# Kernel tuning notes

Measured on AMD Instinct MI355X. Metric: run time of the kernel, lower is better.

Reference implementation:

```python
import jax, jax.numpy as jnp
import numpy as np

EMBED_DIM = 768
Q_DIM = 64
V_DIM = 64
WINDOW_SIZE = 3


def setup_inputs() -> dict:
    key = jax.random.key(0)
    ks = jax.random.split(key, 7)
    B, N = 4, 4096
    s = 1.0 / np.sqrt(EMBED_DIM)
    x = jax.random.normal(ks[0], (B, N, EMBED_DIM), dtype=jnp.float32)
    Wq = jax.random.normal(ks[1], (EMBED_DIM, Q_DIM), dtype=jnp.float32) * s
    bq = jax.random.normal(ks[2], (Q_DIM,), dtype=jnp.float32) * 0.01
    Wk = jax.random.normal(ks[3], (EMBED_DIM, Q_DIM), dtype=jnp.float32) * s
    bk = jax.random.normal(ks[4], (Q_DIM,), dtype=jnp.float32) * 0.01
    Wv = jax.random.normal(ks[5], (EMBED_DIM, V_DIM), dtype=jnp.float32) * s
    bv = jax.random.normal(ks[6], (V_DIM,), dtype=jnp.float32) * 0.01
    return {"x": x, "Wq": Wq, "bq": bq, "Wk": Wk, "bk": bk, "Wv": Wv, "bv": bv}


def reference(x, Wq, bq, Wk, bk, Wv, bv):
    # Faithful translation of SliddingWindowAttention.forward, including the
    # original's quirk: diagonal scores are written into columns 0..window_size-1
    # of a full (B, N, N) zero matrix, softmax is taken over ALL N columns
    # (zeros included), and the result is matmul'd with V.
    B, N, _ = x.shape
    Q = x @ Wq + bq  # (B, N, Q_DIM)
    K = x @ Wk + bk  # (B, N, Q_DIM)
    V = x @ Wv + bv  # (B, N, V_DIM)

    half = WINDOW_SIZE // 2
    columns = jnp.zeros((B, N, N), dtype=x.dtype)
    for idx, di in enumerate(range(-half, half + 1)):
        # diagonal offset di: pair row i with column j = i + di (valid rows only)
        rows = np.arange(max(0, -di), N - max(0, di))
        cols_j = rows + di
        c = jnp.einsum('bid,bid->bi', Q[:, rows, :], K[:, cols_j, :])
        columns = columns.at[:, rows, idx].set(c)

    attn = jax.nn.softmax(columns, axis=2)  # (B, N, N)
    return attn @ V  # (B, N, V_DIM)
```

## Files before the change

kernel.cpp:

```cpp
#include <hip/hip_runtime.h>
#include <math.h>

#define EMBED 768
#define NTOK  4096
#define NB    4
#define ROWS  16384
#define CN    192

typedef __attribute__((ext_vector_type(8))) short bf16x8;
typedef __attribute__((ext_vector_type(8))) unsigned short u16x8;
typedef __attribute__((ext_vector_type(4))) float f32x4;

__device__ inline void split2(float f, short& h, short& l) {
  union { float f; unsigned u; } a; a.f = f;
  unsigned r = (a.u + 0x7FFFu + ((a.u >> 16) & 1u)) & 0xFFFF0000u;
  h = (short)(r >> 16);
  union { unsigned u; float f; } hf; hf.u = r;
  union { float f; unsigned u; } b; b.f = f - hf.f;
  l = (short)((b.u + 0x7FFFu + ((b.u >> 16) & 1u)) >> 16);
}

__device__ inline void splitA(float f, short& h, short& l) {
  union { float f; unsigned u; } a; a.f = f;
  unsigned r = (a.u + 0x7FFFu + ((a.u >> 16) & 1u)) & 0xFFFF0000u;
  h = (short)(r >> 16);
  union { unsigned u; float f; } hf; hf.u = r;
  union { float f; unsigned u; } b; b.f = f - hf.f;
  l = (short)((b.u + 0x8000u) >> 16);
}

__global__ __launch_bounds__(256) void wprep(const float* __restrict__ Wq,
                                             const float* __restrict__ Wk,
                                             const float* __restrict__ Wv,
                                             unsigned short* __restrict__ Wt,
                                             float* __restrict__ Vsum) {
  __shared__ float tile[32 * 64];
  const int b   = blockIdx.x;
  const int mat = b / 24;
  const int ks  = b - mat * 24;
  const float* W = (mat == 0) ? Wq : (mat == 1) ? Wk : Wv;
  const int t = threadIdx.x;

  const float4* src = (const float4*)(W + ks * 2048);
  ((float4*)tile)[t]       = src[t];
  ((float4*)tile)[t + 256] = src[t + 256];
  __syncthreads();

  const int n  = t >> 2;
  const int ko = (t & 3) * 8;
  u16x8 hv, lv;
#pragma unroll
  for (int j = 0; j < 8; ++j) {
    short h, l;
    split2(tile[(ko + j) * 64 + n], h, l);
    hv[j] = (unsigned short)h;
    lv[j] = (unsigned short)l;
  }
  const size_t base = (size_t)ks * 12288 + (size_t)(mat * 64 + n) * 32 + ko;
  *(u16x8*)(Wt + base)        = hv;
  *(u16x8*)(Wt + base + 6144) = lv;

  if (b == 0 && t < NB * 64) Vsum[t] = 0.f;
}

__device__ inline void gload_lds16(const unsigned short* g, unsigned short* l) {
  __builtin_amdgcn_global_load_lds(
      (const __attribute__((address_space(1))) unsigned int*)(g),
      (__attribute__((address_space(3))) unsigned int*)(l),
      16, 0, 0);
}

#define STAGE(LB, KS) do {                                            \
    const unsigned short* _g = Wtu + (size_t)(KS) * 12288 + tid * 8;  \
    unsigned short* _l = (LB) + tid * 8;                              \
    gload_lds16(_g,          _l);                                     \
    gload_lds16(_g + 2048,   _l + 2048);                              \
    gload_lds16(_g + 4096,   _l + 4096);                              \
    gload_lds16(_g + 6144,   _l + 6144);                              \
    gload_lds16(_g + 8192,   _l + 8192);                              \
    gload_lds16(_g + 10240,  _l + 10240);                             \
  } while (0)

#define DO_NT(LBP, NT, ACC) do {                                               \
    bf16x8 _bh = *(const bf16x8*)((LBP) + (NT) * 512);                         \
    bf16x8 _bl = *(const bf16x8*)((LBP) + (NT) * 512 + 6144);                  \
    ACC = __builtin_amdgcn_mfma_f32_16x16x32_bf16(ah, _bh, ACC, 0, 0, 0);      \
    ACC = __builtin_amdgcn_mfma_f32_16x16x32_bf16(ah, _bl, ACC, 0, 0, 0);      \
    ACC = __builtin_amdgcn_mfma_f32_16x16x32_bf16(al, _bh, ACC, 0, 0, 0);      \
  } while (0)

#define COMPUTE(LB, F0, F1) do {                                      \
    bf16x8 ah, al; short _h, _l;                                      \
    splitA((F0).x, _h, _l); ah[0] = _h; al[0] = _l;                   \
    splitA((F0).y, _h, _l); ah[1] = _h; al[1] = _l;                   \
    splitA((F0).z, _h, _l); ah[2] = _h; al[2] = _l;                   \
    splitA((F0).w, _h, _l); ah[3] = _h; al[3] = _l;                   \
    splitA((F1).x, _h, _l); ah[4] = _h; al[4] = _l;                   \
    splitA((F1).y, _h, _l); ah[5] = _h; al[5] = _l;                   \
    splitA((F1).z, _h, _l); ah[6] = _h; al[6] = _l;                   \
    splitA((F1).w, _h, _l); ah[7] = _h; al[7] = _l;                   \
    const unsigned short* _lb = (LB) + lboff;                         \
    DO_NT(_lb, 0, acc0); DO_NT(_lb, 1, acc1); DO_NT(_lb, 2, acc2);    \
    DO_NT(_lb, 3, acc3); DO_NT(_lb, 4, acc4); DO_NT(_lb, 5, acc5);    \
  } while (0)

__global__ __launch_bounds__(256, 2) void qkv_mfma(const float* __restrict__ x,
                                                   const unsigned short* __restrict__ Wtu,
                                                   const float* __restrict__ bq,
                                                   const float* __restrict__ bk,
                                                   const float* __restrict__ bv,
                                                   float* __restrict__ C,
                                                   float* __restrict__ Vsum) {
  __shared__ unsigned short lbuf0[12288];
  __shared__ unsigned short lbuf1[12288];

  const int tid   = threadIdx.x;
  const int lane  = tid & 63;
  const int wm    = (tid >> 6) & 1;
  const int wn    = tid >> 7;
  const int ml    = lane & 15;
  const int q     = lane >> 4;
  const int r0    = blockIdx.x * 32;
  const int nbase = wn * 96;
  const int lboff = (wn * 96 + ml) * 32 + q * 8;

  f32x4 acc0 = {0.f, 0.f, 0.f, 0.f}, acc1 = {0.f, 0.f, 0.f, 0.f},
        acc2 = {0.f, 0.f, 0.f, 0.f}, acc3 = {0.f, 0.f, 0.f, 0.f},
        acc4 = {0.f, 0.f, 0.f, 0.f}, acc5 = {0.f, 0.f, 0.f, 0.f};

  const float* xap = x + (size_t)(r0 + wm * 16 + ml) * EMBED + q * 8;

  STAGE(lbuf0, 0);
  float4 a0 = *(const float4*)xap;
  float4 a1 = *(const float4*)(xap + 4);

  for (int ks = 0; ks < 24; ks += 2) {
    __syncthreads();
    STAGE(lbuf1, ks + 1);
    float4 n0 = *(const float4*)(xap + 32);
    float4 n1 = *(const float4*)(xap + 36);
    COMPUTE(lbuf0, a0, a1);

    __syncthreads();
    if (ks < 22) {
      STAGE(lbuf0, ks + 2);
      float4 m0 = *(const float4*)(xap + 64);
      float4 m1 = *(const float4*)(xap + 68);
      a0 = m0; a1 = m1;
    }
    COMPUTE(lbuf1, n0, n1);
    xap += 64;
  }

#define EPI(NT, ACC) do {                                                   \
    const int n = nbase + (NT) * 16 + ml;                                   \
    const float bias = (n < 64) ? bq[n] : (n < 128) ? bk[n - 64] : bv[n - 128]; \
    const int row = r0 + wm * 16 + q * 4;                                   \
    C[(size_t)(row + 0) * CN + n] = ACC[0] + bias;                          \
    C[(size_t)(row + 1) * CN + n] = ACC[1] + bias;                          \
    C[(size_t)(row + 2) * CN + n] = ACC[2] + bias;                          \
    C[(size_t)(row + 3) * CN + n] = ACC[3] + bias;                          \
  } while (0)

  EPI(0, acc0); EPI(1, acc1); EPI(2, acc2);
  EPI(3, acc3); EPI(4, acc4); EPI(5, acc5);

#define VS(NT, ACC) do {                                                    \
    const int n = nbase + (NT) * 16 + ml;                                   \
    float s = ACC[0] + ACC[1] + ACC[2] + ACC[3] + 4.f * bv[n - 128];        \
    s += __shfl_xor(s, 16, 64);                                             \
    s += __shfl_xor(s, 32, 64);                                             \
    if (q == 0) atomicAdd(&Vsum[(r0 >> 12) * 64 + (n - 128)], s);           \
  } while (0)

  if (wn == 1) {
    VS(2, acc2); VS(3, acc3); VS(4, acc4); VS(5, acc5);
  }
}

__global__ __launch_bounds__(256) void attn_kernel(const float* __restrict__ C,
                                                   const float* __restrict__ Vsum,
                                                   float* __restrict__ out) {
  const int t    = threadIdx.x;
  const int lane = t & 63;
  const int wave = t >> 6;
  const int r = blockIdx.x * 4 + wave;
  const int b = r >> 12;
  const int i = r & (NTOK - 1);

  const float q  = C[(size_t)r * CN + lane];
  const float kc = C[(size_t)r * CN + 64 + lane];
  float km = 0.f, kp = 0.f;
  if (i > 0)        km = C[(size_t)(r - 1) * CN + 64 + lane];
  if (i < NTOK - 1) kp = C[(size_t)(r + 1) * CN + 64 + lane];

  float p0 = q * km, p1 = q * kc, p2 = q * kp;
#pragma unroll
  for (int off = 32; off > 0; off >>= 1) {
    p0 += __shfl_xor(p0, off, 64);
    p1 += __shfl_xor(p1, off, 64);
    p2 += __shfl_xor(p2, off, 64);
  }

  const float s0 = (i > 0) ? p0 : 0.f;
  const float s1 = p1;
  const float s2 = (i < NTOK - 1) ? p2 : 0.f;
  const float m  = fmaxf(fmaxf(s0, s1), fmaxf(s2, 0.f));
  const float e0 = expf(s0 - m);
  const float e1 = expf(s1 - m);
  const float e2 = expf(s2 - m);
  const float ez = expf(-m);
  const float Z  = e0 + e1 + e2 + (float)(NTOK - 3) * ez;

  const size_t vb = ((size_t)b * NTOK) * CN + 128;
  const float v0 = C[vb + lane];
  const float v1 = C[vb + CN + lane];
  const float v2 = C[vb + 2 * (size_t)CN + lane];
  const float vs = Vsum[b * 64 + lane];

  out[(size_t)r * 64 + lane] =
      (e0 * v0 + e1 * v1 + e2 * v2 + ez * (vs - v0 - v1 - v2)) / Z;
}

extern "C" void kernel_launch(void* const* d_in, const int* in_sizes, int n_in,
                              void* d_out, int out_size, void* d_ws, size_t ws_size,
                              hipStream_t stream) {
  const float* x  = (const float*)d_in[0];
  const float* Wq = (const float*)d_in[1];
  const float* bq = (const float*)d_in[2];
  const float* Wk = (const float*)d_in[3];
  const float* bk = (const float*)d_in[4];
  const float* Wv = (const float*)d_in[5];
  const float* bv = (const float*)d_in[6];
  float* out = (float*)d_out;

  float* C    = (float*)d_ws;
  float* Vsum = C + (size_t)ROWS * CN;
  unsigned short* Wt = (unsigned short*)(Vsum + NB * 64);

  wprep<<<72, 256, 0, stream>>>(Wq, Wk, Wv, Wt, Vsum);
  qkv_mfma<<<512, 256, 0, stream>>>(x, Wt, bq, bk, bv, C, Vsum);
  attn_kernel<<<ROWS / 4, 256, 0, stream>>>(C, Vsum, out);
}
```

Before: 128.2 us.

## Re-tile QKV MFMA warps across N, reuse B fragments, use hardware bf16 split

Changes the QKV projection's warp tiling. Each of the 4 waves now covers all 32 rows and 48 output columns, instead of a 2x2 split of 16 rows by 96 columns. Each B fragment loaded from LDS is reused across two A fragments, which roughly halves B LDS reads per MFMA. The weight layout in wprep is reorganized to suit the new LDS offsets. The float-to-bf16 hi/lo split now uses the HIP bf16 conversion intrinsics, with different rounding for the low part than the custom splitA. In exchange, each lane now does twice the x loads and conversions.

```diff
diff --git a/kernel.cpp b/kernel.cpp
--- a/kernel.cpp
+++ b/kernel.cpp
@@ -1,4 +1,5 @@
 #include <hip/hip_runtime.h>
+#include <hip/hip_bf16.h>
 #include <math.h>
 
 #define EMBED 768
@@ -18,15 +19,6 @@
   union { unsigned u; float f; } hf; hf.u = r;
   union { float f; unsigned u; } b; b.f = f - hf.f;
   l = (short)((b.u + 0x7FFFu + ((b.u >> 16) & 1u)) >> 16);
-}
-
-__device__ inline void splitA(float f, short& h, short& l) {
-  union { float f; unsigned u; } a; a.f = f;
-  unsigned r = (a.u + 0x7FFFu + ((a.u >> 16) & 1u)) & 0xFFFF0000u;
-  h = (short)(r >> 16);
-  union { unsigned u; float f; } hf; hf.u = r;
-  union { float f; unsigned u; } b; b.f = f - hf.f;
-  l = (short)((b.u + 0x8000u) >> 16);
 }
 
 __global__ __launch_bounds__(256) void wprep(const float* __restrict__ Wq,
@@ -46,17 +38,17 @@
   ((float4*)tile)[t + 256] = src[t + 256];
   __syncthreads();
 
-  const int n  = t >> 2;
-  const int ko = (t & 3) * 8;
+  const int q    = t >> 6;
+  const int nloc = t & 63;
   u16x8 hv, lv;
 #pragma unroll
   for (int j = 0; j < 8; ++j) {
     short h, l;
-    split2(tile[(ko + j) * 64 + n], h, l);
+    split2(tile[(q * 8 + j) * 64 + nloc], h, l);
     hv[j] = (unsigned short)h;
     lv[j] = (unsigned short)l;
   }
-  const size_t base = (size_t)ks * 12288 + (size_t)(mat * 64 + n) * 32 + ko;
+  const size_t base = (size_t)ks * 12288 + (size_t)q * 1536 + (size_t)(mat * 64 + nloc) * 8;
   *(u16x8*)(Wt + base)        = hv;
   *(u16x8*)(Wt + base + 6144) = lv;
 
@@ -81,27 +73,45 @@
     gload_lds16(_g + 10240,  _l + 10240);                             \
   } while (0)
 
-#define DO_NT(LBP, NT, ACC) do {                                               \
-    bf16x8 _bh = *(const bf16x8*)((LBP) + (NT) * 512);                         \
-    bf16x8 _bl = *(const bf16x8*)((LBP) + (NT) * 512 + 6144);                  \
-    ACC = __builtin_amdgcn_mfma_f32_16x16x32_bf16(ah, _bh, ACC, 0, 0, 0);      \
-    ACC = __builtin_amdgcn_mfma_f32_16x16x32_bf16(ah, _bl, ACC, 0, 0, 0);      \
-    ACC = __builtin_amdgcn_mfma_f32_16x16x32_bf16(al, _bh, ACC, 0, 0, 0);      \
-  } while (0)
-
-#define COMPUTE(LB, F0, F1) do {                                      \
-    bf16x8 ah, al; short _h, _l;                                      \
-    splitA((F0).x, _h, _l); ah[0] = _h; al[0] = _l;                   \
-    splitA((F0).y, _h, _l); ah[1] = _h; al[1] = _l;                   \
-    splitA((F0).z, _h, _l); ah[2] = _h; al[2] = _l;                   \
-    splitA((F0).w, _h, _l); ah[3] = _h; al[3] = _l;                   \
-    splitA((F1).x, _h, _l); ah[4] = _h; al[4] = _l;                   \
-    splitA((F1).y, _h, _l); ah[5] = _h; al[5] = _l;                   \
-    splitA((F1).z, _h, _l); ah[6] = _h; al[6] = _l;                   \
-    splitA((F1).w, _h, _l); ah[7] = _h; al[7] = _l;                   \
-    const unsigned short* _lb = (LB) + lboff;                         \
-    DO_NT(_lb, 0, acc0); DO_NT(_lb, 1, acc1); DO_NT(_lb, 2, acc2);    \
-    DO_NT(_lb, 3, acc3); DO_NT(_lb, 4, acc4); DO_NT(_lb, 5, acc5);    \
+__device__ inline void splitHW(float f, short& h, short& l) {
+  __hip_bfloat16 hb = __float2bfloat16(f);
+  float hf = __bfloat162float(hb);
+  __hip_bfloat16 lb = __float2bfloat16(f - hf);
+  h = __builtin_bit_cast(short, hb);
+  l = __builtin_bit_cast(short, lb);
+}
+
+__device__ inline void cvt8hw(const float4 f0, const float4 f1, bf16x8& h, bf16x8& l) {
+  short hh, ll;
+  splitHW(f0.x, hh, ll); h[0] = hh; l[0] = ll;
+  splitHW(f0.y, hh, ll); h[1] = hh; l[1] = ll;
+  splitHW(f0.z, hh, ll); h[2] = hh; l[2] = ll;
+  splitHW(f0.w, hh, ll); h[3] = hh; l[3] = ll;
+  splitHW(f1.x, hh, ll); h[4] = hh; l[4] = ll;
+  splitHW(f1.y, hh, ll); h[5] = hh; l[5] = ll;
+  splitHW(f1.z, hh, ll); h[6] = hh; l[6] = ll;
+  splitHW(f1.w, hh, ll); h[7] = hh; l[7] = ll;
+}
+
+#define DO_NT3(LBP, NT, ACC0, ACC1) do {                                       \
+    bf16x8 _bh = *(const bf16x8*)((LBP) + (NT) * 128);                         \
+    bf16x8 _bl = *(const bf16x8*)((LBP) + (NT) * 128 + 6144);                  \
+    ACC0 = __builtin_amdgcn_mfma_f32_16x16x32_bf16(ah0, _bh, ACC0, 0, 0, 0);   \
+    ACC0 = __builtin_amdgcn_mfma_f32_16x16x32_bf16(ah0, _bl, ACC0, 0, 0, 0);   \
+    ACC0 = __builtin_amdgcn_mfma_f32_16x16x32_bf16(al0, _bh, ACC0, 0, 0, 0);   \
+    ACC1 = __builtin_amdgcn_mfma_f32_16x16x32_bf16(ah1, _bh, ACC1, 0, 0, 0);   \
+    ACC1 = __builtin_amdgcn_mfma_f32_16x16x32_bf16(ah1, _bl, ACC1, 0, 0, 0);   \
+    ACC1 = __builtin_amdgcn_mfma_f32_16x16x32_bf16(al1, _bh, ACC1, 0, 0, 0);   \
+  } while (0)
+
+#define COMPUTE(LB, A00, A01, A10, A11) do {                          \
+    bf16x8 ah0, al0, ah1, al1;                                        \
+    cvt8hw(A00, A01, ah0, al0);                                       \
+    cvt8hw(A10, A11, ah1, al1);                                       \
+    const unsigned short* _lb = (LB) + lbo;                           \
+    DO_NT3(_lb, 0, acc00, acc10);                                     \
+    DO_NT3(_lb, 1, acc01, acc11);                                     \
+    DO_NT3(_lb, 2, acc02, acc12);                                     \
   } while (0)
 
 __global__ __launch_bounds__(256, 2) void qkv_mfma(const float* __restrict__ x,
@@ -114,68 +124,72 @@
   __shared__ unsigned short lbuf0[12288];
   __shared__ unsigned short lbuf1[12288];
 
-  const int tid   = threadIdx.x;
-  const int lane  = tid & 63;
-  const int wm    = (tid >> 6) & 1;
-  const int wn    = tid >> 7;
-  const int ml    = lane & 15;
-  const int q     = lane >> 4;
-  const int r0    = blockIdx.x * 32;
-  const int nbase = wn * 96;
-  const int lboff = (wn * 96 + ml) * 32 + q * 8;
-
-  f32x4 acc0 = {0.f, 0.f, 0.f, 0.f}, acc1 = {0.f, 0.f, 0.f, 0.f},
-        acc2 = {0.f, 0.f, 0.f, 0.f}, acc3 = {0.f, 0.f, 0.f, 0.f},
-        acc4 = {0.f, 0.f, 0.f, 0.f}, acc5 = {0.f, 0.f, 0.f, 0.f};
-
-  const float* xap = x + (size_t)(r0 + wm * 16 + ml) * EMBED + q * 8;
+  const int tid  = threadIdx.x;
+  const int lane = tid & 63;
+  const int wn   = tid >> 6;
+  const int ml   = lane & 15;
+  const int q    = lane >> 4;
+  const int r0   = blockIdx.x * 32;
+  const int lbo  = q * 1536 + (wn * 48 + ml) * 8;
+
+  f32x4 acc00 = {0.f,0.f,0.f,0.f}, acc01 = {0.f,0.f,0.f,0.f}, acc02 = {0.f,0.f,0.f,0.f};
+  f32x4 acc10 = {0.f,0.f,0.f,0.f}, acc11 = {0.f,0.f,0.f,0.f}, acc12 = {0.f,0.f,0.f,0.f};
+
+  const float* xa0 = x + (size_t)(r0 + ml) * EMBED + q * 8;
+  const float* xa1 = xa0 + (size_t)16 * EMBED;
 
   STAGE(lbuf0, 0);
-  float4 a0 = *(const float4*)xap;
-  float4 a1 = *(const float4*)(xap + 4);
+  float4 a00 = *(const float4*)xa0;
+  float4 a01 = *(const float4*)(xa0 + 4);
+  float4 a10 = *(const float4*)xa1;
+  float4 a11 = *(const float4*)(xa1 + 4);
 
   for (int ks = 0; ks < 24; ks += 2) {
     __syncthreads();
     STAGE(lbuf1, ks + 1);
-    float4 n0 = *(const float4*)(xap + 32);
-    float4 n1 = *(const float4*)(xap + 36);
-    COMPUTE(lbuf0, a0, a1);
+    float4 n00 = *(const float4*)(xa0 + 32);
+    float4 n01 = *(const float4*)(xa0 + 36);
+    float4 n10 = *(const float4*)(xa1 + 32);
+    float4 n11 = *(const float4*)(xa1 + 36);
+    COMPUTE(lbuf0, a00, a01, a10, a11);
 
     __syncthreads();
     if (ks < 22) {
       STAGE(lbuf0, ks + 2);
-      float4 m0 = *(const float4*)(xap + 64);
-      float4 m1 = *(const float4*)(xap + 68);
-      a0 = m0; a1 = m1;
+      a00 = *(const float4*)(xa0 + 64);
+      a01 = *(const float4*)(xa0 + 68);
+      a10 = *(const float4*)(xa1 + 64);
+      a11 = *(const float4*)(xa1 + 68);
     }
-    COMPUTE(lbuf1, n0, n1);
-    xap += 64;
+    COMPUTE(lbuf1, n00, n01, n10, n11);
+    xa0 += 64; xa1 += 64;
   }
 
-#define EPI(NT, ACC) do {                                                   \
-    const int n = nbase + (NT) * 16 + ml;                                   \
+#define EPI(NT, ACC, MF) do {                                               \
+    const int n = wn * 48 + (NT) * 16 + ml;                                 \
     const float bias = (n < 64) ? bq[n] : (n < 128) ? bk[n - 64] : bv[n - 128]; \
-    const int row = r0 + wm * 16 + q * 4;                                   \
+    const int row = r0 + (MF) * 16 + q * 4;                                 \
     C[(size_t)(row + 0) * CN + n] = ACC[0] + bias;                          \
     C[(size_t)(row + 1) * CN + n] = ACC[1] + bias;                          \
     C[(size_t)(row + 2) * CN + n] = ACC[2] + bias;                          \
     C[(size_t)(row + 3) * CN + n] = ACC[3] + bias;                          \
   } while (0)
 
-  EPI(0, acc0); EPI(1, acc1); EPI(2, acc2);
-  EPI(3, acc3); EPI(4, acc4); EPI(5, acc5);
-
-#define VS(NT, ACC) do {                                                    \
-    const int n = nbase + (NT) * 16 + ml;                                   \
-    float s = ACC[0] + ACC[1] + ACC[2] + ACC[3] + 4.f * bv[n - 128];        \
-    s += __shfl_xor(s, 16, 64);                                             \
-    s += __shfl_xor(s, 32, 64);                                             \
-    if (q == 0) atomicAdd(&Vsum[(r0 >> 12) * 64 + (n - 128)], s);           \
-  } while (0)
-
-  if (wn == 1) {
-    VS(2, acc2); VS(3, acc3); VS(4, acc4); VS(5, acc5);
-  }
+  EPI(0, acc00, 0); EPI(1, acc01, 0); EPI(2, acc02, 0);
+  EPI(0, acc10, 1); EPI(1, acc11, 1); EPI(2, acc12, 1);
+
+#define VS(NT, ACC0, ACC1) do {                                             \
+    const int n = wn * 48 + (NT) * 16 + ml;                                 \
+    if (n >= 128) {                                                         \
+      float s = ACC0[0] + ACC0[1] + ACC0[2] + ACC0[3]                       \
+              + ACC1[0] + ACC1[1] + ACC1[2] + ACC1[3] + 8.f * bv[n - 128];  \
+      s += __shfl_xor(s, 16, 64);                                           \
+      s += __shfl_xor(s, 32, 64);                                           \
+      if (q == 0) atomicAdd(&Vsum[(r0 >> 12) * 64 + (n - 128)], s);         \
+    }                                                                       \
+  } while (0)
+
+  VS(0, acc00, acc10); VS(1, acc01, acc11); VS(2, acc02, acc12);
 }
 
 __global__ __launch_bounds__(256) void attn_kernel(const float* __restrict__ C,
```

Measured after the change: 133.5 us. 1.04x slower.
